# Performance work log

Measured on AMD Instinct MI355X. Metric: run time of the kernel, lower is better.

## Reference

```python
import jax, jax.numpy as jnp
import numpy as np

D_K = 64
SCALE = 1.0 / np.sqrt(D_K).astype(np.float32)


def setup_inputs() -> dict:
    key = jax.random.key(0)
    kq, kk, kv = jax.random.split(key, 3)
    B, S, D = 4, 2048, 512
    q = jax.random.normal(kq, (B, S, D), dtype=jnp.float32)
    k = jax.random.normal(kk, (B, S, D), dtype=jnp.float32)
    v = jax.random.normal(kv, (B, S, D), dtype=jnp.float32)
    return {"q": q, "k": k, "v": v}


def reference(q, k, v):
    # n_head == 1: the per-head strided slices are the full tensors.
    # Original computes BOTH 'new_k' (scaled q@k^T) and 'new_v' (unscaled q@k^T);
    # note: v is never used in the original forward math (faithful reproduction).
    qk = jnp.einsum('bsd,btd->bst', q, k)           # [B, S, S]
    scores = qk * SCALE                              # new_k
    attn = jax.nn.softmax(scores, axis=2)            # softmax over dim 2
    # dropout with p=0.1 is identity in eval / deterministic reference
    out = jnp.matmul(attn, qk)                       # attn @ new_v -> [B, S, S]
    return out
```

## Files before the change

kernel.cpp:

```cpp
#include <hip/hip_runtime.h>
#include <hip/hip_bf16.h>
#include <stdint.h>


#define SS 2048
#define DD 512
#define BATCH 4
#define NTB 8

typedef __attribute__((ext_vector_type(8))) short short8;
typedef __attribute__((ext_vector_type(8))) _Float16 half8;
typedef __attribute__((ext_vector_type(4))) float floatx4;
typedef __attribute__((ext_vector_type(4))) float float4v;
typedef __attribute__((ext_vector_type(4))) unsigned int uintx4;

#define GLOBAL_AS const __attribute__((address_space(1)))
#define LDS_AS __attribute__((address_space(3)))

__device__ __forceinline__ float bf2f(uint32_t hbits) {
    union { uint32_t u; float f; } c; c.u = hbits << 16; return c.f;
}
__device__ __forceinline__ uint32_t f2bf_rne(float f) {
    union { float f; uint32_t u; } c; c.f = f;
    return (c.u + 0x7fffu + ((c.u >> 16) & 1u)) >> 16;
}
__device__ __forceinline__ uint32_t pk2h(float x, float y) {
    _Float16 hx = (_Float16)x, hy = (_Float16)y;
    union { _Float16 h; uint16_t u; } cx, cy;
    cx.h = hx; cy.h = hy;
    return (uint32_t)cx.u | ((uint32_t)cy.u << 16);
}

union PackU { uint32_t u[4]; short8 s8; };

__global__ __launch_bounds__(256) void prep_kernel(
    const float* __restrict__ Q, const float* __restrict__ K,
    uint16_t* __restrict__ qT, uint16_t* __restrict__ kB)
{
    const int b   = blockIdx.z;
    const int tid = threadIdx.x;

    if (blockIdx.y == 8) {
        const float* kb_ = K + (size_t)b * SS * DD;
        uint16_t* ob = kB + (size_t)b * SS * DD;
        const int g0 = blockIdx.x * 256 + tid;
#pragma unroll
        for (int i = 0; i < 16; ++i) {
            const int g = g0 + i * 8192;
            const float4v* src = (const float4v*)(kb_ + (size_t)g * 8);
            float4v x0 = src[0], x1 = src[1];
            PackU p;
            p.u[0] = f2bf_rne(x0[0]) | (f2bf_rne(x0[1]) << 16);
            p.u[1] = f2bf_rne(x0[2]) | (f2bf_rne(x0[3]) << 16);
            p.u[2] = f2bf_rne(x1[0]) | (f2bf_rne(x1[1]) << 16);
            p.u[3] = f2bf_rne(x1[2]) | (f2bf_rne(x1[3]) << 16);
            *(short8*)(ob + (size_t)g * 8) = p.s8;
        }
        return;
    }

    const int u0 = blockIdx.x * 64;
    const int d0 = blockIdx.y * 64;
    const float* qb = Q + (size_t)b * SS * DD;
    uint16_t* qTb = qT + (size_t)b * DD * SS;

    __shared__ uint16_t T[64 * 66];

    {
        const int r  = tid >> 2;
        const int c4 = (tid & 3) * 16;
        const float* src = qb + (size_t)(u0 + r) * DD + d0 + c4;
        float4v x0 = *(const float4v*)(src + 0);
        float4v x1 = *(const float4v*)(src + 4);
        float4v x2 = *(const float4v*)(src + 8);
        float4v x3 = *(const float4v*)(src + 12);
        uint32_t w0 = f2bf_rne(x0[0]) | (f2bf_rne(x0[1]) << 16);
        uint32_t w1 = f2bf_rne(x0[2]) | (f2bf_rne(x0[3]) << 16);
        uint32_t w2 = f2bf_rne(x1[0]) | (f2bf_rne(x1[1]) << 16);
        uint32_t w3 = f2bf_rne(x1[2]) | (f2bf_rne(x1[3]) << 16);
        uint32_t w4 = f2bf_rne(x2[0]) | (f2bf_rne(x2[1]) << 16);
        uint32_t w5 = f2bf_rne(x2[2]) | (f2bf_rne(x2[3]) << 16);
        uint32_t w6 = f2bf_rne(x3[0]) | (f2bf_rne(x3[1]) << 16);
        uint32_t w7 = f2bf_rne(x3[2]) | (f2bf_rne(x3[3]) << 16);
        uint32_t* tw = (uint32_t*)&T[r * 66 + c4];
        tw[0] = w0; tw[1] = w1; tw[2] = w2; tw[3] = w3;
        tw[4] = w4; tw[5] = w5; tw[6] = w6; tw[7] = w7;
    }
    __syncthreads();
#pragma unroll
    for (int p = 0; p < 2; ++p) {
        const int dl  = (tid >> 3) + p * 32;
        const int ul8 = (tid & 7) * 8;
        uint16_t t8[8];
#pragma unroll
        for (int j = 0; j < 8; ++j) t8[j] = T[(ul8 + j) * 66 + dl];
        PackU o;
        o.u[0] = (uint32_t)t8[0] | ((uint32_t)t8[1] << 16);
        o.u[1] = (uint32_t)t8[2] | ((uint32_t)t8[3] << 16);
        o.u[2] = (uint32_t)t8[4] | ((uint32_t)t8[5] << 16);
        o.u[3] = (uint32_t)t8[6] | ((uint32_t)t8[7] << 16);
        *(short8*)(&qTb[(size_t)(d0 + dl) * SS + u0 + ul8]) = o.s8;
    }
}

__global__ __launch_bounds__(256, 2) void gemm1_kernel(
    const float* __restrict__ Q, const float* __restrict__ K,
    uint16_t* __restrict__ qk)
{
    const int b  = blockIdx.z;
    const int s0 = blockIdx.y * 128;
    const int t0 = blockIdx.x * 128;
    const float* qb = Q + (size_t)b * SS * DD;
    const float* kb = K + (size_t)b * SS * DD;

    __shared__ uint16_t Ah[2 * 128 * 32];
    __shared__ uint16_t Bh[2 * 128 * 32];

    const int tid  = threadIdx.x;
    const int lane = tid & 63;
    const int wave = tid >> 6;
    const int wm   = wave >> 1;
    const int wn   = wave & 1;
    const int fm   = lane & 15;
    const int quad = lane >> 4;

    floatx4 acc[4][4];
#pragma unroll
    for (int i = 0; i < 4; ++i)
#pragma unroll
        for (int j = 0; j < 4; ++j)
            acc[i][j] = (floatx4)0.0f;

    const int r  = tid >> 1;
    const int c0 = (tid & 1) * 16;
    const float* gA = qb + (size_t)(s0 + r) * DD + c0;
    const float* gB = kb + (size_t)(t0 + r) * DD + c0;

    for (int k0 = 0; k0 < DD; k0 += 64) {
        uint32_t pa[2][8], pb[2][8];
#pragma unroll
        for (int ks = 0; ks < 2; ++ks) {
            float4v a4[4], b4[4];
#pragma unroll
            for (int l = 0; l < 4; ++l) {
                a4[l] = *(const float4v*)(gA + k0 + ks * 32 + l * 4);
                b4[l] = *(const float4v*)(gB + k0 + ks * 32 + l * 4);
            }
#pragma unroll
            for (int l = 0; l < 4; ++l) {
                pa[ks][2 * l]     = pk2h(a4[l][0], a4[l][1]);
                pa[ks][2 * l + 1] = pk2h(a4[l][2], a4[l][3]);
                pb[ks][2 * l]     = pk2h(b4[l][0], b4[l][1]);
                pb[ks][2 * l + 1] = pk2h(b4[l][2], b4[l][3]);
            }
        }
        __syncthreads();
#pragma unroll
        for (int ks = 0; ks < 2; ++ks) {
            PackU p;
            p.u[0]=pa[ks][0]; p.u[1]=pa[ks][1]; p.u[2]=pa[ks][2]; p.u[3]=pa[ks][3];
            *(short8*)(&Ah[ks * 4096 + r * 32 + c0]) = p.s8;
            p.u[0]=pa[ks][4]; p.u[1]=pa[ks][5]; p.u[2]=pa[ks][6]; p.u[3]=pa[ks][7];
            *(short8*)(&Ah[ks * 4096 + r * 32 + c0 + 8]) = p.s8;
            p.u[0]=pb[ks][0]; p.u[1]=pb[ks][1]; p.u[2]=pb[ks][2]; p.u[3]=pb[ks][3];
            *(short8*)(&Bh[ks * 4096 + r * 32 + c0]) = p.s8;
            p.u[0]=pb[ks][4]; p.u[1]=pb[ks][5]; p.u[2]=pb[ks][6]; p.u[3]=pb[ks][7];
            *(short8*)(&Bh[ks * 4096 + r * 32 + c0 + 8]) = p.s8;
        }
        __syncthreads();

#pragma unroll
        for (int ks = 0; ks < 2; ++ks) {
            half8 fa[4], fb[4];
#pragma unroll
            for (int mt = 0; mt < 4; ++mt)
                fa[mt] = *(const half8*)(&Ah[ks * 4096 + (wm * 64 + mt * 16 + fm) * 32 + quad * 8]);
#pragma unroll
            for (int nt = 0; nt < 4; ++nt)
                fb[nt] = *(const half8*)(&Bh[ks * 4096 + (wn * 64 + nt * 16 + fm) * 32 + quad * 8]);
#pragma unroll
            for (int mt = 0; mt < 4; ++mt)
#pragma unroll
                for (int nt = 0; nt < 4; ++nt)
                    acc[mt][nt] = __builtin_amdgcn_mfma_f32_16x16x32_f16(fa[mt], fb[nt], acc[mt][nt], 0, 0, 0);
        }
    }

    uint16_t* qkb = qk + (size_t)b * SS * SS;
#pragma unroll
    for (int mt = 0; mt < 4; ++mt) {
#pragma unroll
        for (int nt = 0; nt < 4; ++nt) {
            const int srow = s0 + wm * 64 + mt * 16 + quad * 4;
            const int tcol = t0 + wn * 64 + nt * 16 + fm;
            qkb[(size_t)(srow + 0) * SS + tcol] = (uint16_t)f2bf_rne(acc[mt][nt][0]);
            qkb[(size_t)(srow + 1) * SS + tcol] = (uint16_t)f2bf_rne(acc[mt][nt][1]);
            qkb[(size_t)(srow + 2) * SS + tcol] = (uint16_t)f2bf_rne(acc[mt][nt][2]);
            qkb[(size_t)(srow + 3) * SS + tcol] = (uint16_t)f2bf_rne(acc[mt][nt][3]);
        }
    }
}

__global__ __launch_bounds__(256) void softmax_inplace(uint16_t* __restrict__ qk)
{
    const size_t row = blockIdx.x;
    uint16_t* x = qk + row * SS;
    const int tid  = threadIdx.x;
    const int lane = tid & 63;
    const int wave = tid >> 6;

    uintx4 raw = *(const uintx4*)(x + tid * 8);
    float v[8];
#pragma unroll
    for (int i = 0; i < 4; ++i) {
        uint32_t u = raw[i];
        v[2 * i]     = bf2f(u & 0xffffu) * 0.125f;
        v[2 * i + 1] = bf2f(u >> 16) * 0.125f;
    }
    float m = v[0];
#pragma unroll
    for (int j = 1; j < 8; ++j) m = fmaxf(m, v[j]);
#pragma unroll
    for (int off = 1; off < 64; off <<= 1) m = fmaxf(m, __shfl_xor(m, off, 64));
    __shared__ float red[8];
    if (lane == 0) red[wave] = m;
    __syncthreads();
    m = fmaxf(fmaxf(red[0], red[1]), fmaxf(red[2], red[3]));

    float s = 0.f;
#pragma unroll
    for (int j = 0; j < 8; ++j) { v[j] = __expf(v[j] - m); s += v[j]; }
#pragma unroll
    for (int off = 1; off < 64; off <<= 1) s += __shfl_xor(s, off, 64);
    if (lane == 0) red[4 + wave] = s;
    __syncthreads();
    s = (red[4] + red[5]) + (red[6] + red[7]);
    const float inv = 1.0f / s;
#pragma unroll
    for (int i = 0; i < 4; ++i)
        raw[i] = f2bf_rne(v[2 * i] * inv) | (f2bf_rne(v[2 * i + 1] * inv) << 16);
    *(uintx4*)(x + tid * 8) = raw;
}

__global__ __launch_bounds__(256, 2) void gemm2a_kernel(
    const uint16_t* __restrict__ attn, const uint16_t* __restrict__ qT,
    uint16_t* __restrict__ tmp)
{
    const int b  = blockIdx.z;
    const int s0 = blockIdx.y * 128;
    const int t0 = blockIdx.x * 128;
    const uint16_t* ab = attn + (size_t)b * SS * SS;
    const uint16_t* bb = qT   + (size_t)b * DD * SS;

    __shared__ uint16_t As[2 * 128 * 32];
    __shared__ uint16_t Bs[2 * 128 * 32];

    const int tid  = threadIdx.x;
    const int lane = tid & 63;
    const int wave = tid >> 6;
    const int wm = wave >> 1, wn = wave & 1;
    const int fm = lane & 15, quad = lane >> 4;

    floatx4 acc[4][4];
#pragma unroll
    for (int i = 0; i < 4; ++i)
#pragma unroll
        for (int j = 0; j < 4; ++j)
            acc[i][j] = (floatx4)0.0f;

    const int c0i = wave * 128 + lane;
    const int c1i = c0i + 64;
    const int rA0 = c0i >> 2, pA0 = c0i & 3;
    const int rA1 = c1i >> 2, pA1 = c1i & 3;
    const int ldsOff0 = (wave * 128) * 8;
    const int ldsOff1 = (wave * 128 + 64) * 8;

    for (int k0 = 0; k0 < SS; k0 += 64) {
        __syncthreads();
#pragma unroll
        for (int ks = 0; ks < 2; ++ks) {
            const int kc = k0 + ks * 32;
            uint16_t* asub = &As[ks * 4096];
            uint16_t* bsub = &Bs[ks * 4096];
            __builtin_amdgcn_global_load_lds(
                (GLOBAL_AS void*)(ab + (size_t)(s0 + rA0) * SS + kc + pA0 * 8),
                (LDS_AS void*)(asub + ldsOff0), 16, 0, 0);
            __builtin_amdgcn_global_load_lds(
                (GLOBAL_AS void*)(ab + (size_t)(s0 + rA1) * SS + kc + pA1 * 8),
                (LDS_AS void*)(asub + ldsOff1), 16, 0, 0);
            __builtin_amdgcn_global_load_lds(
                (GLOBAL_AS void*)(bb + (size_t)(t0 + rA0) * SS + kc + pA0 * 8),
                (LDS_AS void*)(bsub + ldsOff0), 16, 0, 0);
            __builtin_amdgcn_global_load_lds(
                (GLOBAL_AS void*)(bb + (size_t)(t0 + rA1) * SS + kc + pA1 * 8),
                (LDS_AS void*)(bsub + ldsOff1), 16, 0, 0);
        }
        __syncthreads();

#pragma unroll
        for (int ks = 0; ks < 2; ++ks) {
            short8 fa[4], fb[4];
#pragma unroll
            for (int mt = 0; mt < 4; ++mt)
                fa[mt] = *(const short8*)(&As[ks * 4096 + (wm * 64 + mt * 16 + fm) * 32 + quad * 8]);
#pragma unroll
            for (int nt = 0; nt < 4; ++nt)
                fb[nt] = *(const short8*)(&Bs[ks * 4096 + (wn * 64 + nt * 16 + fm) * 32 + quad * 8]);
#pragma unroll
            for (int mt = 0; mt < 4; ++mt)
#pragma unroll
                for (int nt = 0; nt < 4; ++nt)
                    acc[mt][nt] = __builtin_amdgcn_mfma_f32_16x16x32_bf16(fa[mt], fb[nt], acc[mt][nt], 0, 0, 0);
        }
    }

    uint16_t* tb = tmp + (size_t)b * SS * DD;
#pragma unroll
    for (int mt = 0; mt < 4; ++mt) {
#pragma unroll
        for (int nt = 0; nt < 4; ++nt) {
            const int srow = s0 + wm * 64 + mt * 16 + quad * 4;
            const int tcol = t0 + wn * 64 + nt * 16 + fm;
#pragma unroll
            for (int reg = 0; reg < 4; ++reg)
                tb[(size_t)(srow + reg) * DD + tcol] = (uint16_t)f2bf_rne(acc[mt][nt][reg]);
        }
    }
}

__global__ __launch_bounds__(512, 2) void gemm2b_kernel(
    const uint16_t* __restrict__ tmp, const uint16_t* __restrict__ kB,
    float* __restrict__ out)
{
    const int b  = blockIdx.z;
    const int s0 = blockIdx.y * 256;
    const int t0 = blockIdx.x * 256;
    const uint16_t* ab = tmp + (size_t)b * SS * DD;
    const uint16_t* bb = kB  + (size_t)b * SS * DD;

    __shared__ uint16_t smem[65536];

    const int tid  = threadIdx.x;
    const int lane = tid & 63;
    const int wave = tid >> 6;
    const int wm   = wave >> 2;
    const int wn   = wave & 3;
    const int fm   = lane & 15;
    const int quad = lane >> 4;

    floatx4 acc[8][4];
#pragma unroll
    for (int i = 0; i < 8; ++i)
#pragma unroll
        for (int j = 0; j < 4; ++j)
            acc[i][j] = (floatx4)0.0f;

    const int sl0  = (quad ^ (fm & 7)) * 8;
    const int aoff = (wm * 128 + fm) * 64;
    const int boff = 32768 + (wn * 64 + fm) * 64;

    const int c0 = wave * 128 + lane;
    const int r0 = c0 >> 3;  const int l0 = ((c0 & 7) ^ (r0 & 7)) * 8;
    const int c1 = c0 + 64;
    const int r1 = c1 >> 3;  const int l1 = ((c1 & 7) ^ (r1 & 7)) * 8;
    const int ldsW = wave * 1024;

    auto STAGE_A = [&](int tt, int h) {
        uint16_t* base = &smem[(tt & 1) * 16384 + h * 8192 + ldsW];
        __builtin_amdgcn_global_load_lds(
            (GLOBAL_AS void*)(ab + (size_t)(s0 + h * 128 + r0) * DD + tt * 64 + l0),
            (LDS_AS void*)(base), 16, 0, 0);
        __builtin_amdgcn_global_load_lds(
            (GLOBAL_AS void*)(ab + (size_t)(s0 + h * 128 + r1) * DD + tt * 64 + l1),
            (LDS_AS void*)(base + 512), 16, 0, 0);
    };
    auto STAGE_B = [&](int tt, int h) {
        uint16_t* base = &smem[32768 + (tt & 1) * 16384 + h * 8192 + ldsW];
        __builtin_amdgcn_global_load_lds(
            (GLOBAL_AS void*)(bb + (size_t)(t0 + h * 128 + r0) * DD + tt * 64 + l0),
            (LDS_AS void*)(base), 16, 0, 0);
        __builtin_amdgcn_global_load_lds(
            (GLOBAL_AS void*)(bb + (size_t)(t0 + h * 128 + r1) * DD + tt * 64 + l1),
            (LDS_AS void*)(base + 512), 16, 0, 0);
    };

    STAGE_A(0, 0); STAGE_A(0, 1); STAGE_B(0, 0); STAGE_B(0, 1);
    STAGE_B(1, 0); STAGE_B(1, 1);
    asm volatile("s_waitcnt vmcnt(4)" ::: "memory");
    __builtin_amdgcn_s_barrier();

    short8 aF[4], aF2[4], bF[4][2];

    for (int t = 0; t < NTB; ++t) {
        const int abase = (t & 1) * 16384;
        const int bbase = (t & 1) * 16384;

#pragma unroll
        for (int nt = 0; nt < 4; ++nt) {
            bF[nt][0] = *(const short8*)&smem[bbase + boff + nt * 1024 + sl0];
            bF[nt][1] = *(const short8*)&smem[bbase + boff + nt * 1024 + (sl0 ^ 32)];
        }
#pragma unroll
        for (int m = 0; m < 4; ++m)
            aF[m] = *(const short8*)&smem[abase + aoff + m * 1024 + sl0];
        if (t + 1 < NTB) STAGE_A(t + 1, 0);
        __builtin_amdgcn_s_barrier();
        asm volatile("s_waitcnt lgkmcnt(0)" ::: "memory");
        __builtin_amdgcn_s_setprio(1);
#pragma unroll
        for (int m = 0; m < 4; ++m)
#pragma unroll
            for (int nt = 0; nt < 4; ++nt)
                acc[m][nt] = __builtin_amdgcn_mfma_f32_16x16x32_bf16(aF[m], bF[nt][0], acc[m][nt], 0, 0, 0);
        __builtin_amdgcn_s_setprio(0);
        __builtin_amdgcn_s_barrier();

#pragma unroll
        for (int m = 0; m < 4; ++m)
            aF2[m] = *(const short8*)&smem[abase + aoff + (m + 4) * 1024 + sl0];
        if (t + 1 < NTB) STAGE_A(t + 1, 1);
        __builtin_amdgcn_s_barrier();
        asm volatile("s_waitcnt lgkmcnt(0)" ::: "memory");
        __builtin_amdgcn_s_setprio(1);
#pragma unroll
        for (int m = 0; m < 4; ++m)
#pragma unroll
            for (int nt = 0; nt < 4; ++nt)
                acc[m + 4][nt] = __builtin_amdgcn_mfma_f32_16x16x32_bf16(aF2[m], bF[nt][0], acc[m + 4][nt], 0, 0, 0);
        __builtin_amdgcn_s_setprio(0);
        __builtin_amdgcn_s_barrier();

#pragma unroll
        for (int m = 0; m < 4; ++m)
            aF[m] = *(const short8*)&smem[abase + aoff + m * 1024 + (sl0 ^ 32)];
        if (t + 2 < NTB) STAGE_B(t + 2, 0);
        __builtin_amdgcn_s_barrier();
        asm volatile("s_waitcnt lgkmcnt(0)" ::: "memory");
        __builtin_amdgcn_s_setprio(1);
#pragma unroll
        for (int m = 0; m < 4; ++m)
#pragma unroll
            for (int nt = 0; nt < 4; ++nt)
                acc[m][nt] = __builtin_amdgcn_mfma_f32_16x16x32_bf16(aF[m], bF[nt][1], acc[m][nt], 0, 0, 0);
        __builtin_amdgcn_s_setprio(0);
        __builtin_amdgcn_s_barrier();

#pragma unroll
        for (int m = 0; m < 4; ++m)
            aF2[m] = *(const short8*)&smem[abase + aoff + (m + 4) * 1024 + (sl0 ^ 32)];
        if (t + 2 < NTB) {
            STAGE_B(t + 2, 1);
            asm volatile("s_waitcnt vmcnt(4)" ::: "memory");
        } else {
            asm volatile("s_waitcnt vmcnt(0)" ::: "memory");
        }
        __builtin_amdgcn_s_barrier();
        asm volatile("s_waitcnt lgkmcnt(0)" ::: "memory");
        __builtin_amdgcn_s_setprio(1);
#pragma unroll
        for (int m = 0; m < 4; ++m)
#pragma unroll
            for (int nt = 0; nt < 4; ++nt)
                acc[m + 4][nt] = __builtin_amdgcn_mfma_f32_16x16x32_bf16(aF2[m], bF[nt][1], acc[m + 4][nt], 0, 0, 0);
        __builtin_amdgcn_s_setprio(0);
        __builtin_amdgcn_s_barrier();
    }

    float* ob = out + (size_t)b * SS * SS;
#pragma unroll
    for (int mt = 0; mt < 8; ++mt) {
#pragma unroll
        for (int nt = 0; nt < 4; ++nt) {
            const int srow = s0 + wm * 128 + mt * 16 + quad * 4;
            const int tcol = t0 + wn * 64 + nt * 16 + fm;
#pragma unroll
            for (int reg = 0; reg < 4; ++reg)
                ob[(size_t)(srow + reg) * SS + tcol] = acc[mt][nt][reg];
        }
    }
}

extern "C" void kernel_launch(void* const* d_in, const int* in_sizes, int n_in,
                              void* d_out, int out_size, void* d_ws, size_t ws_size,
                              hipStream_t stream) {
    const float* q = (const float*)d_in[0];
    const float* k = (const float*)d_in[1];
    float* out = (float*)d_out;

    uint16_t* qk  = (uint16_t*)d_ws;
    uint16_t* qT  = qk + (size_t)BATCH * SS * SS;
    uint16_t* kB  = qT + (size_t)BATCH * DD * SS;
    uint16_t* tmp = kB + (size_t)BATCH * SS * DD;

    dim3 grid1(SS / 128, SS / 128, BATCH);
    gemm1_kernel<<<grid1, 256, 0, stream>>>(q, k, qk);
    prep_kernel<<<dim3(32, 9, BATCH), 256, 0, stream>>>(q, k, qT, kB);
    softmax_inplace<<<dim3(BATCH * SS), 256, 0, stream>>>(qk);
    gemm2a_kernel<<<dim3(DD / 128, SS / 128, BATCH), 256, 0, stream>>>(qk, qT, tmp);
    gemm2b_kernel<<<dim3(SS / 256, SS / 256, BATCH), 512, 0, stream>>>(tmp, kB, out);
}
```

Before: 225.1 us.

## Pre-convert Q/K to fp16 and reuse pipelined 256x256 GEMM for QK^T

```diff
diff --git a/kernel.cpp b/kernel.cpp
--- a/kernel.cpp
+++ b/kernel.cpp
@@ -17,44 +17,46 @@
 #define GLOBAL_AS const __attribute__((address_space(1)))
 #define LDS_AS __attribute__((address_space(3)))
 
-__device__ __forceinline__ float bf2f(uint32_t hbits) {
-    union { uint32_t u; float f; } c; c.u = hbits << 16; return c.f;
-}
-__device__ __forceinline__ uint32_t f2bf_rne(float f) {
-    union { float f; uint32_t u; } c; c.f = f;
-    return (c.u + 0x7fffu + ((c.u >> 16) & 1u)) >> 16;
-}
 __device__ __forceinline__ uint32_t pk2h(float x, float y) {
     _Float16 hx = (_Float16)x, hy = (_Float16)y;
     union { _Float16 h; uint16_t u; } cx, cy;
     cx.h = hx; cy.h = hy;
     return (uint32_t)cx.u | ((uint32_t)cy.u << 16);
 }
+__device__ __forceinline__ float h2f(uint32_t ubits) {
+    union { uint16_t u; _Float16 h; } c; c.u = (uint16_t)ubits; return (float)c.h;
+}
+__device__ __forceinline__ uint16_t f2h(float f) {
+    union { _Float16 h; uint16_t u; } c; c.h = (_Float16)f; return c.u;
+}
 
 union PackU { uint32_t u[4]; short8 s8; };
 
 __global__ __launch_bounds__(256) void prep_kernel(
     const float* __restrict__ Q, const float* __restrict__ K,
-    uint16_t* __restrict__ qT, uint16_t* __restrict__ kB)
+    uint16_t* __restrict__ qT, uint16_t* __restrict__ qH,
+    uint16_t* __restrict__ kH)
 {
     const int b   = blockIdx.z;
     const int tid = threadIdx.x;
 
-    if (blockIdx.y == 8) {
-        const float* kb_ = K + (size_t)b * SS * DD;
-        uint16_t* ob = kB + (size_t)b * SS * DD;
+    if (blockIdx.y >= 8) {
+        const float* src = (blockIdx.y == 8) ? (K + (size_t)b * SS * DD)
+                                             : (Q + (size_t)b * SS * DD);
+        uint16_t* dst = (blockIdx.y == 8) ? (kH + (size_t)b * SS * DD)
+                                          : (qH + (size_t)b * SS * DD);
         const int g0 = blockIdx.x * 256 + tid;
 #pragma unroll
         for (int i = 0; i < 16; ++i) {
             const int g = g0 + i * 8192;
-            const float4v* src = (const float4v*)(kb_ + (size_t)g * 8);
-            float4v x0 = src[0], x1 = src[1];
+            const float4v* s4 = (const float4v*)(src + (size_t)g * 8);
+            float4v x0 = s4[0], x1 = s4[1];
             PackU p;
-            p.u[0] = f2bf_rne(x0[0]) | (f2bf_rne(x0[1]) << 16);
-            p.u[1] = f2bf_rne(x0[2]) | (f2bf_rne(x0[3]) << 16);
-            p.u[2] = f2bf_rne(x1[0]) | (f2bf_rne(x1[1]) << 16);
-            p.u[3] = f2bf_rne(x1[2]) | (f2bf_rne(x1[3]) << 16);
-            *(short8*)(ob + (size_t)g * 8) = p.s8;
+            p.u[0] = pk2h(x0[0], x0[1]);
+            p.u[1] = pk2h(x0[2], x0[3]);
+            p.u[2] = pk2h(x1[0], x1[1]);
+            p.u[3] = pk2h(x1[2], x1[3]);
+            *(short8*)(dst + (size_t)g * 8) = p.s8;
         }
         return;
     }
@@ -74,17 +76,11 @@
         float4v x1 = *(const float4v*)(src + 4);
         float4v x2 = *(const float4v*)(src + 8);
         float4v x3 = *(const float4v*)(src + 12);
-        uint32_t w0 = f2bf_rne(x0[0]) | (f2bf_rne(x0[1]) << 16);
-        uint32_t w1 = f2bf_rne(x0[2]) | (f2bf_rne(x0[3]) << 16);
-        uint32_t w2 = f2bf_rne(x1[0]) | (f2bf_rne(x1[1]) << 16);
-        uint32_t w3 = f2bf_rne(x1[2]) | (f2bf_rne(x1[3]) << 16);
-        uint32_t w4 = f2bf_rne(x2[0]) | (f2bf_rne(x2[1]) << 16);
-        uint32_t w5 = f2bf_rne(x2[2]) | (f2bf_rne(x2[3]) << 16);
-        uint32_t w6 = f2bf_rne(x3[0]) | (f2bf_rne(x3[1]) << 16);
-        uint32_t w7 = f2bf_rne(x3[2]) | (f2bf_rne(x3[3]) << 16);
         uint32_t* tw = (uint32_t*)&T[r * 66 + c4];
-        tw[0] = w0; tw[1] = w1; tw[2] = w2; tw[3] = w3;
-        tw[4] = w4; tw[5] = w5; tw[6] = w6; tw[7] = w7;
+        tw[0] = pk2h(x0[0], x0[1]); tw[1] = pk2h(x0[2], x0[3]);
+        tw[2] = pk2h(x1[0], x1[1]); tw[3] = pk2h(x1[2], x1[3]);
+        tw[4] = pk2h(x2[0], x2[1]); tw[5] = pk2h(x2[2], x2[3]);
+        tw[6] = pk2h(x3[0], x3[1]); tw[7] = pk2h(x3[2], x3[3]);
     }
     __syncthreads();
 #pragma unroll
@@ -103,100 +99,154 @@
     }
 }
 
-__global__ __launch_bounds__(256, 2) void gemm1_kernel(
-    const float* __restrict__ Q, const float* __restrict__ K,
+__global__ __launch_bounds__(512, 2) void gemm1_kernel(
+    const uint16_t* __restrict__ qH, const uint16_t* __restrict__ kH,
     uint16_t* __restrict__ qk)
 {
     const int b  = blockIdx.z;
-    const int s0 = blockIdx.y * 128;
-    const int t0 = blockIdx.x * 128;
-    const float* qb = Q + (size_t)b * SS * DD;
-    const float* kb = K + (size_t)b * SS * DD;
-
-    __shared__ uint16_t Ah[2 * 128 * 32];
-    __shared__ uint16_t Bh[2 * 128 * 32];
+    const int s0 = blockIdx.y * 256;
+    const int t0 = blockIdx.x * 256;
+    const uint16_t* ab = qH + (size_t)b * SS * DD;
+    const uint16_t* bb = kH + (size_t)b * SS * DD;
+
+    __shared__ uint16_t smem[65536];
 
     const int tid  = threadIdx.x;
     const int lane = tid & 63;
     const int wave = tid >> 6;
-    const int wm   = wave >> 1;
-    const int wn   = wave & 1;
+    const int wm   = wave >> 2;
+    const int wn   = wave & 3;
     const int fm   = lane & 15;
     const int quad = lane >> 4;
 
-    floatx4 acc[4][4];
-#pragma unroll
-    for (int i = 0; i < 4; ++i)
+    floatx4 acc[8][4];
+#pragma unroll
+    for (int i = 0; i < 8; ++i)
 #pragma unroll
         for (int j = 0; j < 4; ++j)
             acc[i][j] = (floatx4)0.0f;
 
-    const int r  = tid >> 1;
-    const int c0 = (tid & 1) * 16;
-    const float* gA = qb + (size_t)(s0 + r) * DD + c0;
-    const float* gB = kb + (size_t)(t0 + r) * DD + c0;
-
-    for (int k0 = 0; k0 < DD; k0 += 64) {
-        uint32_t pa[2][8], pb[2][8];
-#pragma unroll
-        for (int ks = 0; ks < 2; ++ks) {
-            float4v a4[4], b4[4];
-#pragma unroll
-            for (int l = 0; l < 4; ++l) {
-                a4[l] = *(const float4v*)(gA + k0 + ks * 32 + l * 4);
-                b4[l] = *(const float4v*)(gB + k0 + ks * 32 + l * 4);
-            }
-#pragma unroll
-            for (int l = 0; l < 4; ++l) {
-                pa[ks][2 * l]     = pk2h(a4[l][0], a4[l][1]);
-                pa[ks][2 * l + 1] = pk2h(a4[l][2], a4[l][3]);
-                pb[ks][2 * l]     = pk2h(b4[l][0], b4[l][1]);
-                pb[ks][2 * l + 1] = pk2h(b4[l][2], b4[l][3]);
-            }
-        }
-        __syncthreads();
-#pragma unroll
-        for (int ks = 0; ks < 2; ++ks) {
-            PackU p;
-            p.u[0]=pa[ks][0]; p.u[1]=pa[ks][1]; p.u[2]=pa[ks][2]; p.u[3]=pa[ks][3];
-            *(short8*)(&Ah[ks * 4096 + r * 32 + c0]) = p.s8;
-            p.u[0]=pa[ks][4]; p.u[1]=pa[ks][5]; p.u[2]=pa[ks][6]; p.u[3]=pa[ks][7];
-            *(short8*)(&Ah[ks * 4096 + r * 32 + c0 + 8]) = p.s8;
-            p.u[0]=pb[ks][0]; p.u[1]=pb[ks][1]; p.u[2]=pb[ks][2]; p.u[3]=pb[ks][3];
-            *(short8*)(&Bh[ks * 4096 + r * 32 + c0]) = p.s8;
-            p.u[0]=pb[ks][4]; p.u[1]=pb[ks][5]; p.u[2]=pb[ks][6]; p.u[3]=pb[ks][7];
-            *(short8*)(&Bh[ks * 4096 + r * 32 + c0 + 8]) = p.s8;
-        }
-        __syncthreads();
-
-#pragma unroll
-        for (int ks = 0; ks < 2; ++ks) {
-            half8 fa[4], fb[4];
-#pragma unroll
-            for (int mt = 0; mt < 4; ++mt)
-                fa[mt] = *(const half8*)(&Ah[ks * 4096 + (wm * 64 + mt * 16 + fm) * 32 + quad * 8]);
-#pragma unroll
-            for (int nt = 0; nt < 4; ++nt)
-                fb[nt] = *(const half8*)(&Bh[ks * 4096 + (wn * 64 + nt * 16 + fm) * 32 + quad * 8]);
-#pragma unroll
-            for (int mt = 0; mt < 4; ++mt)
-#pragma unroll
-                for (int nt = 0; nt < 4; ++nt)
-                    acc[mt][nt] = __builtin_amdgcn_mfma_f32_16x16x32_f16(fa[mt], fb[nt], acc[mt][nt], 0, 0, 0);
-        }
-    }
-
-    uint16_t* qkb = qk + (size_t)b * SS * SS;
-#pragma unroll
-    for (int mt = 0; mt < 4; ++mt) {
+    const int sl0  = (quad ^ (fm & 7)) * 8;
+    const int aoff = (wm * 128 + fm) * 64;
+    const int boff = 32768 + (wn * 64 + fm) * 64;
+
+    const int c0 = wave * 128 + lane;
+    const int r0 = c0 >> 3;  const int l0 = ((c0 & 7) ^ (r0 & 7)) * 8;
+    const int c1 = c0 + 64;
+    const int r1 = c1 >> 3;  const int l1 = ((c1 & 7) ^ (r1 & 7)) * 8;
+    const int ldsW = wave * 1024;
+
+    auto STAGE_A = [&](int tt, int h) {
+        uint16_t* base = &smem[(tt & 1) * 16384 + h * 8192 + ldsW];
+        __builtin_amdgcn_global_load_lds(
+            (GLOBAL_AS void*)(ab + (size_t)(s0 + h * 128 + r0) * DD + tt * 64 + l0),
+            (LDS_AS void*)(base), 16, 0, 0);
+        __builtin_amdgcn_global_load_lds(
+            (GLOBAL_AS void*)(ab + (size_t)(s0 + h * 128 + r1) * DD + tt * 64 + l1),
+            (LDS_AS void*)(base + 512), 16, 0, 0);
+    };
+    auto STAGE_B = [&](int tt, int h) {
+        uint16_t* base = &smem[32768 + (tt & 1) * 16384 + h * 8192 + ldsW];
+        __builtin_amdgcn_global_load_lds(
+            (GLOBAL_AS void*)(bb + (size_t)(t0 + h * 128 + r0) * DD + tt * 64 + l0),
+            (LDS_AS void*)(base), 16, 0, 0);
+        __builtin_amdgcn_global_load_lds(
+            (GLOBAL_AS void*)(bb + (size_t)(t0 + h * 128 + r1) * DD + tt * 64 + l1),
+            (LDS_AS void*)(base + 512), 16, 0, 0);
+    };
+
+    STAGE_A(0, 0); STAGE_A(0, 1); STAGE_B(0, 0); STAGE_B(0, 1);
+    STAGE_B(1, 0); STAGE_B(1, 1);
+    asm volatile("s_waitcnt vmcnt(4)" ::: "memory");
+    __builtin_amdgcn_s_barrier();
+
+    half8 aF[4], aF2[4], bF[4][2];
+
+    for (int t = 0; t < NTB; ++t) {
+        const int abase = (t & 1) * 16384;
+        const int bbase = (t & 1) * 16384;
+
 #pragma unroll
         for (int nt = 0; nt < 4; ++nt) {
-            const int srow = s0 + wm * 64 + mt * 16 + quad * 4;
+            bF[nt][0] = *(const half8*)&smem[bbase + boff + nt * 1024 + sl0];
+            bF[nt][1] = *(const half8*)&smem[bbase + boff + nt * 1024 + (sl0 ^ 32)];
+        }
+#pragma unroll
+        for (int m = 0; m < 4; ++m)
+            aF[m] = *(const half8*)&smem[abase + aoff + m * 1024 + sl0];
+        if (t + 1 < NTB) STAGE_A(t + 1, 0);
+        __builtin_amdgcn_s_barrier();
+        asm volatile("s_waitcnt lgkmcnt(0)" ::: "memory");
+        __builtin_amdgcn_s_setprio(1);
+#pragma unroll
+        for (int m = 0; m < 4; ++m)
+#pragma unroll
+            for (int nt = 0; nt < 4; ++nt)
+                acc[m][nt] = __builtin_amdgcn_mfma_f32_16x16x32_f16(aF[m], bF[nt][0], acc[m][nt], 0, 0, 0);
+        __builtin_amdgcn_s_setprio(0);
+        __builtin_amdgcn_s_barrier();
+
+#pragma unroll
+        for (int m = 0; m < 4; ++m)
+            aF2[m] = *(const half8*)&smem[abase + aoff + (m + 4) * 1024 + sl0];
+        if (t + 1 < NTB) STAGE_A(t + 1, 1);
+        __builtin_amdgcn_s_barrier();
+        asm volatile("s_waitcnt lgkmcnt(0)" ::: "memory");
+        __builtin_amdgcn_s_setprio(1);
+#pragma unroll
+        for (int m = 0; m < 4; ++m)
+#pragma unroll
+            for (int nt = 0; nt < 4; ++nt)
+                acc[m + 4][nt] = __builtin_amdgcn_mfma_f32_16x16x32_f16(aF2[m], bF[nt][0], acc[m + 4][nt], 0, 0, 0);
+        __builtin_amdgcn_s_setprio(0);
+        __builtin_amdgcn_s_barrier();
+
+#pragma unroll
+        for (int m = 0; m < 4; ++m)
+            aF[m] = *(const half8*)&smem[abase + aoff + m * 1024 + (sl0 ^ 32)];
+        if (t + 2 < NTB) STAGE_B(t + 2, 0);
+        __builtin_amdgcn_s_barrier();
+        asm volatile("s_waitcnt lgkmcnt(0)" ::: "memory");
+        __builtin_amdgcn_s_setprio(1);
+#pragma unroll
+        for (int m = 0; m < 4; ++m)
+#pragma unroll
+            for (int nt = 0; nt < 4; ++nt)
+                acc[m][nt] = __builtin_amdgcn_mfma_f32_16x16x32_f16(aF[m], bF[nt][1], acc[m][nt], 0, 0, 0);
+        __builtin_amdgcn_s_setprio(0);
+        __builtin_amdgcn_s_barrier();
+
+#pragma unroll
+        for (int m = 0; m < 4; ++m)
+            aF2[m] = *(const half8*)&smem[abase + aoff + (m + 4) * 1024 + (sl0 ^ 32)];
+        if (t + 2 < NTB) {
+            STAGE_B(t + 2, 1);
+            asm volatile("s_waitcnt vmcnt(4)" ::: "memory");
+        } else {
+            asm volatile("s_waitcnt vmcnt(0)" ::: "memory");
+        }
+        __builtin_amdgcn_s_barrier();
+        asm volatile("s_waitcnt lgkmcnt(0)" ::: "memory");
+        __builtin_amdgcn_s_setprio(1);
+#pragma unroll
+        for (int m = 0; m < 4; ++m)
+#pragma unroll
+            for (int nt = 0; nt < 4; ++nt)
+                acc[m + 4][nt] = __builtin_amdgcn_mfma_f32_16x16x32_f16(aF2[m], bF[nt][1], acc[m + 4][nt], 0, 0, 0);
+        __builtin_amdgcn_s_setprio(0);
+        __builtin_amdgcn_s_barrier();
+    }
+
+    uint16_t* ob = qk + (size_t)b * SS * SS;
+#pragma unroll
+    for (int mt = 0; mt < 8; ++mt) {
+#pragma unroll
+        for (int nt = 0; nt < 4; ++nt) {
+            const int srow = s0 + wm * 128 + mt * 16 + quad * 4;
             const int tcol = t0 + wn * 64 + nt * 16 + fm;
-            qkb[(size_t)(srow + 0) * SS + tcol] = (uint16_t)f2bf_rne(acc[mt][nt][0]);
-            qkb[(size_t)(srow + 1) * SS + tcol] = (uint16_t)f2bf_rne(acc[mt][nt][1]);
-            qkb[(size_t)(srow + 2) * SS + tcol] = (uint16_t)f2bf_rne(acc[mt][nt][2]);
-            qkb[(size_t)(srow + 3) * SS + tcol] = (uint16_t)f2bf_rne(acc[mt][nt][3]);
+#pragma unroll
+            for (int reg = 0; reg < 4; ++reg)
+                ob[(size_t)(srow + reg) * SS + tcol] = f2h(acc[mt][nt][reg]);
         }
     }
 }
@@ -214,8 +264,8 @@
 #pragma unroll
     for (int i = 0; i < 4; ++i) {
         uint32_t u = raw[i];
-        v[2 * i]     = bf2f(u & 0xffffu) * 0.125f;
-        v[2 * i + 1] = bf2f(u >> 16) * 0.125f;
+        v[2 * i]     = h2f(u & 0xffffu) * 0.125f;
+        v[2 * i + 1] = h2f(u >> 16) * 0.125f;
     }
     float m = v[0];
 #pragma unroll
@@ -238,7 +288,7 @@
     const float inv = 1.0f / s;
 #pragma unroll
     for (int i = 0; i < 4; ++i)
-        raw[i] = f2bf_rne(v[2 * i] * inv) | (f2bf_rne(v[2 * i + 1] * inv) << 16);
+        raw[i] = pk2h(v[2 * i] * inv, v[2 * i + 1] * inv);
     *(uintx4*)(x + tid * 8) = raw;
 }
 
@@ -299,18 +349,18 @@
 
 #pragma unroll
         for (int ks = 0; ks < 2; ++ks) {
-            short8 fa[4], fb[4];
+            half8 fa[4], fb[4];
 #pragma unroll
             for (int mt = 0; mt < 4; ++mt)
-                fa[mt] = *(const short8*)(&As[ks * 4096 + (wm * 64 + mt * 16 + fm) * 32 + quad * 8]);
-#pragma unroll
-            for (int nt = 0; nt < 4; ++nt)
-                fb[nt] = *(const short8*)(&Bs[ks * 4096 + (wn * 64 + nt * 16 + fm) * 32 + quad * 8]);
+                fa[mt] = *(const half8*)(&As[ks * 4096 + (wm * 64 + mt * 16 + fm) * 32 + quad * 8]);
+#pragma unroll
+            for (int nt = 0; nt < 4; ++nt)
+                fb[nt] = *(const half8*)(&Bs[ks * 4096 + (wn * 64 + nt * 16 + fm) * 32 + quad * 8]);
 #pragma unroll
             for (int mt = 0; mt < 4; ++mt)
 #pragma unroll
                 for (int nt = 0; nt < 4; ++nt)
-                    acc[mt][nt] = __builtin_amdgcn_mfma_f32_16x16x32_bf16(fa[mt], fb[nt], acc[mt][nt], 0, 0, 0);
+                    acc[mt][nt] = __builtin_amdgcn_mfma_f32_16x16x32_f16(fa[mt], fb[nt], acc[mt][nt], 0, 0, 0);
         }
     }
 
@@ -323,20 +373,20 @@
             const int tcol = t0 + wn * 64 + nt * 16 + fm;
 #pragma unroll
             for (int reg = 0; reg < 4; ++reg)
-                tb[(size_t)(srow + reg) * DD + tcol] = (uint16_t)f2bf_rne(acc[mt][nt][reg]);
+                tb[(size_t)(srow + reg) * DD + tcol] = f2h(acc[mt][nt][reg]);
         }
     }
 }
 
 __global__ __launch_bounds__(512, 2) void gemm2b_kernel(
-    const uint16_t* __restrict__ tmp, const uint16_t* __restrict__ kB,
+    const uint16_t* __restrict__ tmp, const uint16_t* __restrict__ kH,
     float* __restrict__ out)
 {
     const int b  = blockIdx.z;
     const int s0 = blockIdx.y * 256;
     const int t0 = blockIdx.x * 256;
     const uint16_t* ab = tmp + (size_t)b * SS * DD;
-    const uint16_t* bb = kB  + (size_t)b * SS * DD;
+    const uint16_t* bb = kH  + (size_t)b * SS * DD;
 
     __shared__ uint16_t smem[65536];
 
@@ -389,7 +439,7 @@
     asm volatile("s_waitcnt vmcnt(4)" ::: "memory");
     __builtin_amdgcn_s_barrier();
 
-    short8 aF[4], aF2[4], bF[4][2];
+    half8 aF[4], aF2[4], bF[4][2];
 
     for (int t = 0; t < NTB; ++t) {
         const int abase = (t & 1) * 16384;
@@ -397,12 +447,12 @@
 
 #pragma unroll
         for (int nt = 0; nt < 4; ++nt) {
-            bF[nt][0] = *(const short8*)&smem[bbase + boff + nt * 1024 + sl0];
-            bF[nt][1] = *(const short8*)&smem[bbase + boff + nt * 1024 + (sl0 ^ 32)];
-        }
-#pragma unroll
-        for (int m = 0; m < 4; ++m)
-            aF[m] = *(const short8*)&smem[abase + aoff + m * 1024 + sl0];
+            bF[nt][0] = *(const half8*)&smem[bbase + boff + nt * 1024 + sl0];
+            bF[nt][1] = *(const half8*)&smem[bbase + boff + nt * 1024 + (sl0 ^ 32)];
+        }
+#pragma unroll
+        for (int m = 0; m < 4; ++m)
+            aF[m] = *(const half8*)&smem[abase + aoff + m * 1024 + sl0];
         if (t + 1 < NTB) STAGE_A(t + 1, 0);
         __builtin_amdgcn_s_barrier();
         asm volatile("s_waitcnt lgkmcnt(0)" ::: "memory");
@@ -411,13 +461,13 @@
         for (int m = 0; m < 4; ++m)
 #pragma unroll
             for (int nt = 0; nt < 4; ++nt)
-                acc[m][nt] = __builtin_amdgcn_mfma_f32_16x16x32_bf16(aF[m], bF[nt][0], acc[m][nt], 0, 0, 0);
-        __builtin_amdgcn_s_setprio(0);
-        __builtin_amdgcn_s_barrier();
-
-#pragma unroll
-        for (int m = 0; m < 4; ++m)
-            aF2[m] = *(const short8*)&smem[abase + aoff + (m + 4) * 1024 + sl0];
+                acc[m][nt] = __builtin_amdgcn_mfma_f32_16x16x32_f16(aF[m], bF[nt][0], acc[m][nt], 0, 0, 0);
+        __builtin_amdgcn_s_setprio(0);
+        __builtin_amdgcn_s_barrier();
+
+#pragma unroll
+        for (int m = 0; m < 4; ++m)
+            aF2[m] = *(const half8*)&smem[abase + aoff + (m + 4) * 1024 + sl0];
         if (t + 1 < NTB) STAGE_A(t + 1, 1);
         __builtin_amdgcn_s_barrier();
         asm volatile("s_waitcnt lgkmcnt(0)" ::: "memory");
@@ -426,13 +476,13 @@
         for (int m = 0; m < 4; ++m)
 #pragma unroll
             for (int nt = 0; nt < 4; ++nt)
-                acc[m + 4][nt] = __builtin_amdgcn_mfma_f32_16x16x32_bf16(aF2[m], bF[nt][0], acc[m + 4][nt], 0, 0, 0);
-        __builtin_amdgcn_s_setprio(0);
-        __builtin_amdgcn_s_barrier();
-
-#pragma unroll
-        for (int m = 0; m < 4; ++m)
-            aF[m] = *(const short8*)&smem[abase + aoff + m * 1024 + (sl0 ^ 32)];
+                acc[m + 4][nt] = __builtin_amdgcn_mfma_f32_16x16x32_f16(aF2[m], bF[nt][0], acc[m + 4][nt], 0, 0, 0);
+        __builtin_amdgcn_s_setprio(0);
+        __builtin_amdgcn_s_barrier();
+
+#pragma unroll
+        for (int m = 0; m < 4; ++m)
+            aF[m] = *(const half8*)&smem[abase + aoff + m * 1024 + (sl0 ^ 32)];
         if (t + 2 < NTB) STAGE_B(t + 2, 0);
         __builtin_amdgcn_s_barrier();
         asm volatile("s_waitcnt lgkmcnt(0)" ::: "memory");
@@ -441,13 +491,13 @@
         for (int m = 0; m < 4; ++m)
 #pragma unroll
             for (int nt = 0; nt < 4; ++nt)
-                acc[m][nt] = __builtin_amdgcn_mfma_f32_16x16x32_bf16(aF[m], bF[nt][1], acc[m][nt], 0, 0, 0);
-        __builtin_amdgcn_s_setprio(0);
-        __builtin_amdgcn_s_barrier();
-
-#pragma unroll
-        for (int m = 0; m < 4; ++m)
-            aF2[m] = *(const short8*)&smem[abase + aoff + (m + 4) * 1024 + (sl0 ^ 32)];
+                acc[m][nt] = __builtin_amdgcn_mfma_f32_16x16x32_f16(aF[m], bF[nt][1], acc[m][nt], 0, 0, 0);
+        __builtin_amdgcn_s_setprio(0);
+        __builtin_amdgcn_s_barrier();
+
+#pragma unroll
+        for (int m = 0; m < 4; ++m)
+            aF2[m] = *(const half8*)&smem[abase + aoff + (m + 4) * 1024 + (sl0 ^ 32)];
         if (t + 2 < NTB) {
             STAGE_B(t + 2, 1);
             asm volatile("s_waitcnt vmcnt(4)" ::: "memory");
@@ -461,7 +511,7 @@
         for (int m = 0; m < 4; ++m)
 #pragma unroll
             for (int nt = 0; nt < 4; ++nt)
-                acc[m + 4][nt] = __builtin_amdgcn_mfma_f32_16x16x32_bf16(aF2[m], bF[nt][1], acc[m + 4][nt], 0, 0, 0);
+                acc[m + 4][nt] = __builtin_amdgcn_mfma_f32_16x16x32_f16(aF2[m], bF[nt][1], acc[m + 4][nt], 0, 0, 0);
         __builtin_amdgcn_s_setprio(0);
         __builtin_amdgcn_s_barrier();
     }
@@ -489,13 +539,13 @@
 
     uint16_t* qk  = (uint16_t*)d_ws;
     uint16_t* qT  = qk + (size_t)BATCH * SS * SS;
-    uint16_t* kB  = qT + (size_t)BATCH * DD * SS;
-    uint16_t* tmp = kB + (size_t)BATCH * SS * DD;
-
-    dim3 grid1(SS / 128, SS / 128, BATCH);
-    gemm1_kernel<<<grid1, 256, 0, stream>>>(q, k, qk);
-    prep_kernel<<<dim3(32, 9, BATCH), 256, 0, stream>>>(q, k, qT, kB);
+    uint16_t* qH  = qT + (size_t)BATCH * DD * SS;
+    uint16_t* kH  = qH + (size_t)BATCH * SS * DD;
+    uint16_t* tmp = kH + (size_t)BATCH * SS * DD;
+
+    prep_kernel<<<dim3(32, 10, BATCH), 256, 0, stream>>>(q, k, qT, qH, kH);
+    gemm1_kernel<<<dim3(SS / 256, SS / 256, BATCH), 512, 0, stream>>>(qH, kH, qk);
     softmax_inplace<<<dim3(BATCH * SS), 256, 0, stream>>>(qk);
     gemm2a_kernel<<<dim3(DD / 128, SS / 128, BATCH), 256, 0, stream>>>(qk, qT, tmp);
-    gemm2b_kernel<<<dim3(SS / 256, SS / 256, BATCH), 512, 0, stream>>>(tmp, kB, out);
-}
+    gemm2b_kernel<<<dim3(SS / 256, SS / 256, BATCH), 512, 0, stream>>>(tmp, kH, out);
+}
```

New measurement: 204.9 us. -8.9%, faster.
